# Optimization experiments

Measured on AMD Instinct MI355X. Metric: run time of the kernel, lower is better.

Reference implementation:

```python
import jax, jax.numpy as jnp
import numpy as np

KERNEL = 7
STRIDE = 1
DILATION = 1


def _unfold(x, k, d, pad, stride):
    """torch.nn.Unfold semantics on NCHW input -> [n, c, k*k, oh*ow]."""
    n, c, H, W = x.shape
    eff = d * (k - 1) + 1
    oh = (H + 2 * pad - eff) // stride + 1
    ow = (W + 2 * pad - eff) // stride + 1
    xp = jnp.pad(x, ((0, 0), (0, 0), (pad, pad), (pad, pad)))
    # k*k static slices of the padded map, each strided to the output grid
    cols = [
        xp[:, :, i * d : i * d + (oh - 1) * stride + 1 : stride,
              j * d : j * d + (ow - 1) * stride + 1 : stride]
        for i in range(k) for j in range(k)
    ]
    return jnp.stack(cols, axis=2).reshape(n, c, k * k, oh * ow)


def setup_inputs() -> dict:
    key = jax.random.key(0)
    k1, k2 = jax.random.split(key)
    input1 = jax.random.normal(k1, (8, 32, 112, 112), dtype=jnp.float32)
    input2 = jax.random.normal(k2, (8, 32, 112, 112), dtype=jnp.float32)
    return {"input1": input1, "input2": input2}


def reference(input1, input2):
    n, c, H, W = input1.shape
    pad = (DILATION * (KERNEL - 1) + 1) // 2  # module derives its own zero padding
    eff = DILATION * (KERNEL - 1) + 1
    oh = (H + 2 * pad - eff) // STRIDE + 1
    ow = (W + 2 * pad - eff) // STRIDE + 1
    # unfold_i: kernel=1, padding=0 -> strided center samples, shape [n,c,1,L]
    ui = _unfold(input1, 1, DILATION, 0, STRIDE)  # [n, c, 1, H'*W']
    uj = _unfold(input2, KERNEL, DILATION, pad, STRIDE)  # [n, c, k*k, oh*ow]
    # broadcast subtraction: center feature minus each of the k^2 neighbors
    return ui.reshape(n, c, 1, oh * ow) - uj
```

## Files before the change

### kernel.cpp

```cpp
#include <hip/hip_runtime.h>


#define NC_TOT   256
#define HW       112
#define PLANE    12544
#define X4       28
#define THREADS_TOT (NC_TOT * HW * X4)

__global__ __launch_bounds__(256) void sub2_kernel(
    const float* __restrict__ in1,
    const float* __restrict__ in2,
    float* __restrict__ out)
{
    int t = blockIdx.x * blockDim.x + threadIdx.x;
    if (t >= THREADS_TOT) return;

    int x4 = t % X4;
    int ry = t / X4;
    int y  = ry % HW;
    int nc = ry / HW;
    int x0 = x4 * 4;

    const float4 a = *reinterpret_cast<const float4*>(
        in1 + (size_t)(nc * HW + y) * HW + x0);

    const float* b2 = in2 + (size_t)nc * PLANE;
    float* po = out + (size_t)nc * 49 * PLANE + (size_t)y * HW + x0;

    #pragma unroll
    for (int i = 0; i < 7; ++i) {
        int iy = y + i - 3;
        float w[10];
        if (iy >= 0 && iy < HW) {
            const float* pr = b2 + iy * HW;
            #pragma unroll
            for (int m = 0; m < 10; ++m) {
                int wx = x0 - 3 + m;
                w[m] = (wx >= 0 && wx < HW) ? pr[wx] : 0.0f;
            }
        } else {
            #pragma unroll
            for (int m = 0; m < 10; ++m) w[m] = 0.0f;
        }
        #pragma unroll
        for (int j = 0; j < 7; ++j) {
            float4 r;
            r.x = a.x - w[j + 0];
            r.y = a.y - w[j + 1];
            r.z = a.z - w[j + 2];
            r.w = a.w - w[j + 3];
            *reinterpret_cast<float4*>(po + (size_t)(i * 7 + j) * PLANE) = r;
        }
    }
}

extern "C" void kernel_launch(void* const* d_in, const int* in_sizes, int n_in,
                              void* d_out, int out_size, void* d_ws, size_t ws_size,
                              hipStream_t stream) {
    const float* in1 = (const float*)d_in[0];
    const float* in2 = (const float*)d_in[1];
    float* out = (float*)d_out;

    const int threads = 256;
    const int blocks = (THREADS_TOT + threads - 1) / threads;
    sub2_kernel<<<blocks, threads, 0, stream>>>(in1, in2, out);
}
```

Before: 134.7 us.

## Assign one output plane per block with contiguous nontemporal stores

Restructures the grid so each block writes one full contiguous output plane (one nc, one of the 49 offsets) instead of each thread scattering 49 float4 stores across planes. Each thread handles 7 rows of that plane, reloading the center input and the shifted neighbor values, and writes with nontemporal stores. This is meant to make write streams contiguous per block and reduce cache pollution from the large output, at the cost of reading the inputs about 49 times (mostly from cache).

```diff
diff --git a/kernel.cpp b/kernel.cpp
--- a/kernel.cpp
+++ b/kernel.cpp
@@ -1,56 +1,57 @@
 #include <hip/hip_runtime.h>
 
 
-#define NC_TOT   256
-#define HW       112
-#define PLANE    12544
-#define X4       28
-#define THREADS_TOT (NC_TOT * HW * X4)
+#define NC_TOT 256
+#define HW     112
+#define PLANE  12544
+#define KK     49
 
-__global__ __launch_bounds__(256) void sub2_kernel(
+typedef float f4 __attribute__((ext_vector_type(4)));
+
+__global__ __launch_bounds__(448) void sub2_plane_kernel(
     const float* __restrict__ in1,
     const float* __restrict__ in2,
     float* __restrict__ out)
 {
-    int t = blockIdx.x * blockDim.x + threadIdx.x;
-    if (t >= THREADS_TOT) return;
+    const int b  = blockIdx.x;
+    const int nc = b & 255;
+    const int p  = b >> 8;
+    const int dy = p / 7 - 3;
+    const int dx = p % 7 - 3;
 
-    int x4 = t % X4;
-    int ry = t / X4;
-    int y  = ry % HW;
-    int nc = ry / HW;
-    int x0 = x4 * 4;
+    const float* a_pl = in1 + (size_t)nc * PLANE;
+    const float* b_pl = in2 + (size_t)nc * PLANE;
+    float*       o_pl = out + ((size_t)nc * KK + p) * PLANE;
 
-    const float4 a = *reinterpret_cast<const float4*>(
-        in1 + (size_t)(nc * HW + y) * HW + x0);
-
-    const float* b2 = in2 + (size_t)nc * PLANE;
-    float* po = out + (size_t)nc * 49 * PLANE + (size_t)y * HW + x0;
+    const int tid = threadIdx.x;
+    const int y0  = tid / 28;
+    const int x0  = (tid % 28) * 4;
 
     #pragma unroll
-    for (int i = 0; i < 7; ++i) {
-        int iy = y + i - 3;
-        float w[10];
+    for (int k = 0; k < 7; ++k) {
+        const int y = y0 + k * 16;
+        const f4 a = *reinterpret_cast<const f4*>(a_pl + y * HW + x0);
+
+        float w[4] = {0.f, 0.f, 0.f, 0.f};
+        const int iy = y + dy;
         if (iy >= 0 && iy < HW) {
-            const float* pr = b2 + iy * HW;
+            const float* row = b_pl + iy * HW;
+            const int xb = x0 + dx;
             #pragma unroll
-            for (int m = 0; m < 10; ++m) {
-                int wx = x0 - 3 + m;
-                w[m] = (wx >= 0 && wx < HW) ? pr[wx] : 0.0f;
+            for (int m = 0; m < 4; ++m) {
+                const int xx = xb + m;
+                const int xc = xx < 0 ? 0 : (xx > HW - 1 ? HW - 1 : xx);
+                const float v = row[xc];
+                w[m] = (xx >= 0 && xx < HW) ? v : 0.f;
             }
-        } else {
-            #pragma unroll
-            for (int m = 0; m < 10; ++m) w[m] = 0.0f;
         }
-        #pragma unroll
-        for (int j = 0; j < 7; ++j) {
-            float4 r;
-            r.x = a.x - w[j + 0];
-            r.y = a.y - w[j + 1];
-            r.z = a.z - w[j + 2];
-            r.w = a.w - w[j + 3];
-            *reinterpret_cast<float4*>(po + (size_t)(i * 7 + j) * PLANE) = r;
-        }
+
+        f4 r;
+        r.x = a.x - w[0];
+        r.y = a.y - w[1];
+        r.z = a.z - w[2];
+        r.w = a.w - w[3];
+        __builtin_nontemporal_store(r, reinterpret_cast<f4*>(o_pl + y * HW + x0));
     }
 }
 
@@ -61,7 +62,6 @@
     const float* in2 = (const float*)d_in[1];
     float* out = (float*)d_out;
 
-    const int threads = 256;
-    const int blocks = (THREADS_TOT + threads - 1) / threads;
-    sub2_kernel<<<blocks, threads, 0, stream>>>(in1, in2, out);
+    const int blocks = KK * NC_TOT;
+    sub2_plane_kernel<<<blocks, 448, 0, stream>>>(in1, in2, out);
 }
```

Result: slower. 172.3 us (+27.9%).
